# Optimization experiments

Hardware: AMD Instinct MI355X
Metric: run time of the kernel (lower is better)

## Reference

```python
import jax, jax.numpy as jnp
import numpy as np

B, D, O, K = 8192, 256, 256, 16


def setup_inputs() -> dict:
    key = jax.random.key(0)
    k1, k2, k3, k4 = jax.random.split(key, 4)
    x = jax.random.normal(k1, (B, D), dtype=jnp.float32)
    # learned params
    values = jax.random.uniform(k2, (O, D, K), dtype=jnp.float32, minval=-0.05, maxval=0.05)
    skip_w = jax.random.normal(k3, (O, D), dtype=jnp.float32) * (1.0 / np.sqrt(D))
    skip_b = jax.random.uniform(k4, (O,), dtype=jnp.float32, minval=-1.0, maxval=1.0) / np.sqrt(D)
    # fixed buffer (non-trainable)
    grid = jnp.linspace(-1.0, 1.0, K).astype(jnp.float32)
    return {"x": x, "values": values, "skip_w": skip_w, "skip_b": skip_b, "grid": grid}


def reference(x, values, skip_w, skip_b, grid):
    # x: [B, D]; values: [O, D, K]; grid: [K]
    num_knots = grid.shape[0]
    xc = jnp.clip(x, -1.0, 1.0)
    # torch.bucketize(x, grid) (right=False) == searchsorted side='left'
    right = jnp.searchsorted(grid, xc, side="left")            # [B, D]
    left = jnp.clip(right - 1, 0, num_knots - 2)               # [B, D]
    right = left + 1
    g0 = grid[left]
    g1 = grid[right]
    w = (xc - g0) / (g1 - g0 + 1e-12)                          # [B, D]
    # sparse linear-interp coefficients over knots: 2 nonzeros per (b, d)
    coeff = (1.0 - w)[..., None] * jax.nn.one_hot(left, num_knots, dtype=xc.dtype) \
          + w[..., None] * jax.nn.one_hot(right, num_knots, dtype=xc.dtype)  # [B, D, K]
    # y[b,o] = sum_d sum_k coeff[b,d,k] * values[o,d,k]  (== per-dim gather+interp+accumulate)
    y = jnp.einsum("bdk,odk->bo", coeff, values)
    y = y + xc @ skip_w.T + skip_b
    return y
```

## Files before the change

kernel.cpp:

```cpp
#include <hip/hip_runtime.h>
#include <hip/hip_bf16.h>
#include <stdint.h>


#define D_DIM  256
#define O_DIM  256
#define BM     64
#define BK     64
#define KS     4
#define ITERS  16
#define NTHR   256

typedef __attribute__((ext_vector_type(8))) short bf16x8;
typedef __attribute__((ext_vector_type(4))) float f32x4;

__global__ __launch_bounds__(256) void kan_prep(
    const float* __restrict__ values,
    const float* __restrict__ skip_w,
    const float* __restrict__ gknots,
    const float* __restrict__ x,
    unsigned short* __restrict__ Vp)
{
    int tid = blockIdx.x * blockDim.x + threadIdx.x;
    int e = tid * 8;
    int o = e >> 12;
    int kflat = e & 4095;
    float sw = skip_w[(o << 8) | (kflat >> 4)];
    int kmod = kflat & 15;

    const float4* vp4 = reinterpret_cast<const float4*>(values + e);
    float4 v0 = vp4[0], v1 = vp4[1];
    float f[8] = {v0.x, v0.y, v0.z, v0.w, v1.x, v1.y, v1.z, v1.w};
    unsigned int w[4];
#pragma unroll
    for (int j = 0; j < 4; ++j) {
        float2 ab;
        ab.x = f[2*j]     + gknots[kmod + 2*j]     * sw;
        ab.y = f[2*j + 1] + gknots[kmod + 2*j + 1] * sw;
        __hip_bfloat162 p2 = __float22bfloat162_rn(ab);
        __builtin_memcpy(&w[j], &p2, 4);
    }
    size_t c = (size_t)(kflat >> 3) * 256 + (size_t)o;
    *reinterpret_cast<uint4*>(Vp + c * 8) = make_uint4(w[0], w[1], w[2], w[3]);

    {
        int pb = (int)blockIdx.x;
        int mt = (pb & 7) + 8 * ((pb >> 3) & 15);
        int rowbase = mt * BM + (pb >> 7) * 16;
        int t = (int)threadIdx.x;
        const float4* xw = reinterpret_cast<const float4*>(
            x + (size_t)(rowbase + (t >> 4)) * D_DIM) + (t & 15) * 4;
        float s = 0.f;
#pragma unroll
        for (int k = 0; k < 4; ++k) {
            float4 v = xw[k];
            s += v.x + v.y + v.z + v.w;
        }
        asm volatile("" :: "v"(s));
    }
}

__global__ __launch_bounds__(NTHR, 2) void kan_gemm(
    const float* __restrict__ x,
    const unsigned short* __restrict__ Vp,
    float* __restrict__ part,
    float* __restrict__ out)
{
    __shared__ unsigned short As[4][2][64 * 64];

    const int t    = threadIdx.x;
    const int lane = t & 63;
    const int wid  = t >> 6;
    const int l15  = lane & 15;
    const int lhi  = lane >> 4;

    const int bid = (int)blockIdx.x;
    const int m8  = bid & 7;
    const int ks  = (bid >> 3) & 3;
    const int mhi = bid >> 5;
    const int mt  = m8 + 8 * mhi;
    const int bm0 = mt * BM;
    const size_t kc0 = (size_t)ks * 128;

    const float* xr = x + (size_t)(bm0 + lane) * D_DIM + ks * 64;

    char* abase[2] = { (char*)&As[wid][0][0] + lane * 128,
                       (char*)&As[wid][1][0] + lane * 128 };
    const int lsw = lane & 7;

    auto stageA = [&](int buf, float4 xv) {
        float vv[4] = {xv.x, xv.y, xv.z, xv.w};
        char* base = abase[buf];
#pragma unroll
        for (int d = 0; d < 4; ++d) {
            float xc = fminf(1.f, fmaxf(-1.f, vv[d]));
            float tt = (xc + 1.f) * 7.5f;
            int li = (int)tt;
            li = li > 14 ? 14 : li;
            float w1 = tt - (float)li;
            float2 cw; cw.x = 1.f - w1; cw.y = w1;
            __hip_bfloat162 p2 = __float22bfloat162_rn(cw);
            unsigned int pk;
            __builtin_memcpy(&pk, &p2, 4);
            unsigned long long w64 = (unsigned long long)pk << ((li & 1) * 16);
            unsigned int lo = (unsigned int)w64;
            unsigned int hi = (unsigned int)(w64 >> 32);
            int jl = li >> 1;
            unsigned int wd[8];
#pragma unroll
            for (int j = 0; j < 8; ++j)
                wd[j] = (j == jl) ? lo : ((j == jl + 1) ? hi : 0u);
            *reinterpret_cast<uint4*>(base + (((2 * d)     ^ lsw) << 4)) =
                make_uint4(wd[0], wd[1], wd[2], wd[3]);
            *reinterpret_cast<uint4*>(base + (((2 * d + 1) ^ lsw) << 4)) =
                make_uint4(wd[4], wd[5], wd[6], wd[7]);
        }
    };

    #define LOADB(BG, KT)                                                      \
        {                                                                      \
            const unsigned short* _b =                                         \
                Vp + (kc0 + (size_t)(KT) * 8) * 2048;                          \
            _Pragma("unroll")                                                  \
            for (int kh = 0; kh < 2; ++kh)                                     \
                _Pragma("unroll")                                              \
                for (int ni = 0; ni < 4; ++ni) {                               \
                    int n = wid * 64 + ni * 16 + l15;                          \
                    BG[kh * 4 + ni] = *reinterpret_cast<const bf16x8*>(        \
                        _b + ((size_t)((kh * 4 + lhi) * 256 + n)) * 8);        \
                }                                                              \
        }

    f32x4 acc[4][4] = {};
    bf16x8 bgA[8], bgB[8], bgC[8];

    int abyte[4];
#pragma unroll
    for (int mi = 0; mi < 4; ++mi) abyte[mi] = (mi * 16 + l15) * 128;
    const int a7 = l15 & 7;

    float4 xcur = *reinterpret_cast<const float4*>(xr);
    LOADB(bgA, 0)
    LOADB(bgB, 1)
    stageA(0, xcur);
    float4 xn = *reinterpret_cast<const float4*>(xr + 4);

    #define IT(KT, CUR, BGC_, BGN2)                                            \
        {                                                                      \
            const bool last = (KT) == ITERS - 1;                               \
            if ((KT) + 2 < ITERS) { LOADB(BGN2, (KT) + 2) }                    \
            const char* Ab = (const char*)&As[wid][CUR][0];                    \
            bf16x8 af[4];                                                      \
                                                                   \
            _Pragma("unroll")                                                  \
            for (int mi = 0; mi < 4; ++mi)                                     \
                af[mi] = *reinterpret_cast<const bf16x8*>(                     \
                    Ab + abyte[mi] + ((lhi ^ a7) << 4));                       \
            __builtin_amdgcn_s_setprio(1);                                     \
            _Pragma("unroll")                                                  \
            for (int mi = 0; mi < 4; ++mi)                                     \
                _Pragma("unroll")                                              \
                for (int ni = 0; ni < 4; ++ni)                                 \
                    acc[mi][ni] = __builtin_amdgcn_mfma_f32_16x16x32_bf16(     \
                        af[mi], BGC_[ni], acc[mi][ni], 0, 0, 0);               \
            __builtin_amdgcn_s_setprio(0);                                     \
                                    \
            if (!last) {                                                       \
                stageA((CUR) ^ 1, xn);                                         \
                if ((KT) + 2 < ITERS)                                          \
                    xn = *reinterpret_cast<const float4*>(xr + ((KT) + 2) * 4);\
            }                                                                  \
                                                                   \
            _Pragma("unroll")                                                  \
            for (int mi = 0; mi < 4; ++mi)                                     \
                af[mi] = *reinterpret_cast<const bf16x8*>(                     \
                    Ab + abyte[mi] + (((4 + lhi) ^ a7) << 4));                 \
            __builtin_amdgcn_s_setprio(1);                                     \
            _Pragma("unroll")                                                  \
            for (int mi = 0; mi < 4; ++mi)                                     \
                _Pragma("unroll")                                              \
                for (int ni = 0; ni < 4; ++ni)                                 \
                    acc[mi][ni] = __builtin_amdgcn_mfma_f32_16x16x32_bf16(     \
                        af[mi], BGC_[4 + ni], acc[mi][ni], 0, 0, 0);           \
            __builtin_amdgcn_s_setprio(0);                                     \
        }

    IT(0, 0, bgA, bgC)  IT(1, 1, bgB, bgA)  IT(2, 0, bgC, bgB)
    IT(3, 1, bgA, bgC)  IT(4, 0, bgB, bgA)  IT(5, 1, bgC, bgB)
    IT(6, 0, bgA, bgC)  IT(7, 1, bgB, bgA)  IT(8, 0, bgC, bgB)
    IT(9, 1, bgA, bgC)  IT(10, 0, bgB, bgA) IT(11, 1, bgC, bgB)
    IT(12, 0, bgA, bgC) IT(13, 1, bgB, bgA) IT(14, 0, bgC, bgB)
    IT(15, 1, bgA, bgC)
    #undef IT
    #undef LOADB

    float* dst = (ks == 0) ? out : part + (size_t)(ks - 1) * (8192 * 256);
#pragma unroll
    for (int ni = 0; ni < 4; ++ni) {
        int col = wid * 64 + ni * 16 + l15;
#pragma unroll
        for (int mi = 0; mi < 4; ++mi) {
            f32x4 v = acc[mi][ni];
            int row0 = bm0 + mi * 16 + lhi * 4;
#pragma unroll
            for (int r = 0; r < 4; ++r)
                dst[(size_t)(row0 + r) * O_DIM + col] = v[r];
        }
    }
}

__global__ __launch_bounds__(256) void kan_reduce(
    const float* __restrict__ part,
    const float* __restrict__ skip_b,
    float* __restrict__ out)
{
    int rbid = (int)blockIdx.x;
    int c    = rbid & 7;
    int tq   = rbid >> 3;
    int mhi  = tq >> 4;
    int sub  = tq & 15;
    int mt   = c + 8 * mhi;
    int row0 = mt * BM + sub * 4;

    int i   = (int)threadIdx.x;
    int row = row0 + (i >> 6);
    int col = (i & 63) * 4;
    size_t e = (size_t)row * O_DIM + col;

    f32x4 s = *reinterpret_cast<const f32x4*>(out + e);
    s += *reinterpret_cast<const f32x4*>(skip_b + col);
    s += *reinterpret_cast<const f32x4*>(part + e);
    s += *reinterpret_cast<const f32x4*>(part + (size_t)8192 * 256 + e);
    s += *reinterpret_cast<const f32x4*>(part + (size_t)2 * 8192 * 256 + e);
    *reinterpret_cast<f32x4*>(out + e) = s;
}

__global__ __launch_bounds__(256) void kan_naive(
    const float* __restrict__ x,
    const unsigned short* __restrict__ Vp,
    const float* __restrict__ skip_b,
    float* __restrict__ out)
{
    int b = blockIdx.x, o = threadIdx.x;
    float acc = skip_b[o];
    for (int d = 0; d < 256; ++d) {
        float xc = fminf(1.f, fmaxf(-1.f, x[(size_t)b * 256 + d]));
        float tt = (xc + 1.f) * 7.5f;
        int li = (int)tt; li = li > 14 ? 14 : li;
        float w1 = tt - (float)li;
        int k0 = d * 16 + li;
        unsigned short u0 = Vp[((size_t)(k0 >> 3) * 256 + o) * 8 + (k0 & 7)];
        int k1 = k0 + 1;
        unsigned short u1 = Vp[((size_t)(k1 >> 3) * 256 + o) * 8 + (k1 & 7)];
        float f0 = __uint_as_float((unsigned)u0 << 16);
        float f1 = __uint_as_float((unsigned)u1 << 16);
        acc += (1.f - w1) * f0 + w1 * f1;
    }
    out[(size_t)b * 256 + o] = acc;
}

extern "C" void kernel_launch(void* const* d_in, const int* in_sizes, int n_in,
                              void* d_out, int out_size, void* d_ws, size_t ws_size,
                              hipStream_t stream) {
    const float* x      = (const float*)d_in[0];
    const float* values = (const float*)d_in[1];
    const float* skip_w = (const float*)d_in[2];
    const float* skip_b = (const float*)d_in[3];
    const float* gknots = (const float*)d_in[4];
    float* out = (float*)d_out;
    (void)in_sizes; (void)n_in; (void)out_size;

    unsigned short* Vp = (unsigned short*)d_ws;
    float* part = (float*)((char*)d_ws + 2u * 1024 * 1024);

    kan_prep<<<dim3(512), dim3(256), 0, stream>>>(values, skip_w, gknots, x, Vp);

    const size_t need = 2u * 1024 * 1024
                      + (size_t)3 * 8192 * 256 * sizeof(float);
    if (ws_size >= need) {
        kan_gemm<<<dim3(512), dim3(NTHR), 0, stream>>>(x, Vp, part, out);
        kan_reduce<<<dim3(2048), dim3(256), 0, stream>>>(part, skip_b, out);
    } else {
        kan_naive<<<dim3(8192), dim3(256), 0, stream>>>(x, Vp, skip_b, out);
    }
}
```

Baseline: 42.13 us.

## Build interpolation A-fragments directly in registers instead of staging through LDS

Each lane now loads the x values it needs for its own MFMA A-fragment rows and builds the sparse bf16 interpolation coefficients in registers. This removes the shared-memory staging buffer, the LDS writes and reads, and the per-row lane mapping. The cost is redundant coefficient work, since several lanes recompute fragments from the same x elements. Global x loads become four strided rows per lane, and the occupancy hint is dropped from the launch bounds.

Result: slower. 75.70 us (+79.7%).

```diff
diff --git a/kernel.cpp b/kernel.cpp
--- a/kernel.cpp
+++ b/kernel.cpp
@@ -6,7 +6,6 @@
 #define D_DIM  256
 #define O_DIM  256
 #define BM     64
-#define BK     64
 #define KS     4
 #define ITERS  16
 #define NTHR   256
@@ -60,19 +59,19 @@
     }
 }
 
-__global__ __launch_bounds__(NTHR, 2) void kan_gemm(
+__global__ __launch_bounds__(NTHR) void kan_gemm(
     const float* __restrict__ x,
     const unsigned short* __restrict__ Vp,
     float* __restrict__ part,
     float* __restrict__ out)
 {
-    __shared__ unsigned short As[4][2][64 * 64];
-
     const int t    = threadIdx.x;
     const int lane = t & 63;
     const int wid  = t >> 6;
     const int l15  = lane & 15;
     const int lhi  = lane >> 4;
+    const int hi2  = lhi >> 1;
+    const int jbase = (lhi & 1) * 4;
 
     const int bid = (int)blockIdx.x;
     const int m8  = bid & 7;
@@ -82,39 +81,33 @@
     const int bm0 = mt * BM;
     const size_t kc0 = (size_t)ks * 128;
 
-    const float* xr = x + (size_t)(bm0 + lane) * D_DIM + ks * 64;
-
-    char* abase[2] = { (char*)&As[wid][0][0] + lane * 128,
-                       (char*)&As[wid][1][0] + lane * 128 };
-    const int lsw = lane & 7;
-
-    auto stageA = [&](int buf, float4 xv) {
-        float vv[4] = {xv.x, xv.y, xv.z, xv.w};
-        char* base = abase[buf];
-#pragma unroll
-        for (int d = 0; d < 4; ++d) {
-            float xc = fminf(1.f, fmaxf(-1.f, vv[d]));
-            float tt = (xc + 1.f) * 7.5f;
-            int li = (int)tt;
-            li = li > 14 ? 14 : li;
-            float w1 = tt - (float)li;
-            float2 cw; cw.x = 1.f - w1; cw.y = w1;
-            __hip_bfloat162 p2 = __float22bfloat162_rn(cw);
-            unsigned int pk;
-            __builtin_memcpy(&pk, &p2, 4);
-            unsigned long long w64 = (unsigned long long)pk << ((li & 1) * 16);
-            unsigned int lo = (unsigned int)w64;
-            unsigned int hi = (unsigned int)(w64 >> 32);
-            int jl = li >> 1;
-            unsigned int wd[8];
-#pragma unroll
-            for (int j = 0; j < 8; ++j)
-                wd[j] = (j == jl) ? lo : ((j == jl + 1) ? hi : 0u);
-            *reinterpret_cast<uint4*>(base + (((2 * d)     ^ lsw) << 4)) =
-                make_uint4(wd[0], wd[1], wd[2], wd[3]);
-            *reinterpret_cast<uint4*>(base + (((2 * d + 1) ^ lsw) << 4)) =
-                make_uint4(wd[4], wd[5], wd[6], wd[7]);
-        }
+    const float* xrow[4];
+#pragma unroll
+    for (int mi = 0; mi < 4; ++mi)
+        xrow[mi] = x + (size_t)(bm0 + mi * 16 + l15) * D_DIM + ks * 64;
+
+    auto mkfrag = [&](float xv) -> bf16x8 {
+        float xc = fminf(1.f, fmaxf(-1.f, xv));
+        float tt = (xc + 1.f) * 7.5f;
+        int li = (int)tt;
+        li = li > 14 ? 14 : li;
+        float w1 = tt - (float)li;
+        float2 cw; cw.x = 1.f - w1; cw.y = w1;
+        __hip_bfloat162 p2 = __float22bfloat162_rn(cw);
+        unsigned int pk;
+        __builtin_memcpy(&pk, &p2, 4);
+        unsigned long long w64 = (unsigned long long)pk << ((li & 1) << 4);
+        unsigned int lo = (unsigned int)w64;
+        unsigned int hi = (unsigned int)(w64 >> 32);
+        int jl = (li >> 1) - jbase;
+        uint4 w;
+        w.x = (jl == 0) ? lo : ((jl == -1) ? hi : 0u);
+        w.y = (jl == 1) ? lo : ((jl == 0)  ? hi : 0u);
+        w.z = (jl == 2) ? lo : ((jl == 1)  ? hi : 0u);
+        w.w = (jl == 3) ? lo : ((jl == 2)  ? hi : 0u);
+        bf16x8 r;
+        __builtin_memcpy(&r, &w, 16);
+        return r;
     };
 
     #define LOADB(BG, KT)                                                      \
@@ -131,31 +124,30 @@
                 }                                                              \
         }
 
+    #define LOADX(XV, KT)                                                      \
+        {                                                                      \
+            _Pragma("unroll")                                                  \
+            for (int mi = 0; mi < 4; ++mi)                                     \
+                XV[mi] = *reinterpret_cast<const float4*>(xrow[mi] + (KT) * 4);\
+        }
+
     f32x4 acc[4][4] = {};
     bf16x8 bgA[8], bgB[8], bgC[8];
-
-    int abyte[4];
-#pragma unroll
-    for (int mi = 0; mi < 4; ++mi) abyte[mi] = (mi * 16 + l15) * 128;
-    const int a7 = l15 & 7;
-
-    float4 xcur = *reinterpret_cast<const float4*>(xr);
+    float4 xA[4], xB[4];
+
     LOADB(bgA, 0)
     LOADB(bgB, 1)
-    stageA(0, xcur);
-    float4 xn = *reinterpret_cast<const float4*>(xr + 4);
-
-    #define IT(KT, CUR, BGC_, BGN2)                                            \
+    LOADX(xA, 0)
+    LOADX(xB, 1)
+
+    #define IT(KT, BGC_, BGN2, XC, XN)                                         \
         {                                                                      \
-            const bool last = (KT) == ITERS - 1;                               \
             if ((KT) + 2 < ITERS) { LOADB(BGN2, (KT) + 2) }                    \
-            const char* Ab = (const char*)&As[wid][CUR][0];                    \
             bf16x8 af[4];                                                      \
-                                                                   \
-            _Pragma("unroll")                                                  \
-            for (int mi = 0; mi < 4; ++mi)                                     \
-                af[mi] = *reinterpret_cast<const bf16x8*>(                     \
-                    Ab + abyte[mi] + ((lhi ^ a7) << 4));                       \
+                                                   \
+            _Pragma("unroll")                                                  \
+            for (int mi = 0; mi < 4; ++mi)                                     \
+                af[mi] = mkfrag(hi2 ? XC[mi].y : XC[mi].x);                    \
             __builtin_amdgcn_s_setprio(1);                                     \
             _Pragma("unroll")                                                  \
             for (int mi = 0; mi < 4; ++mi)                                     \
@@ -164,17 +156,11 @@
                     acc[mi][ni] = __builtin_amdgcn_mfma_f32_16x16x32_bf16(     \
                         af[mi], BGC_[ni], acc[mi][ni], 0, 0, 0);               \
             __builtin_amdgcn_s_setprio(0);                                     \
-                                    \
-            if (!last) {                                                       \
-                stageA((CUR) ^ 1, xn);                                         \
-                if ((KT) + 2 < ITERS)                                          \
-                    xn = *reinterpret_cast<const float4*>(xr + ((KT) + 2) * 4);\
-            }                                                                  \
-                                                                   \
-            _Pragma("unroll")                                                  \
-            for (int mi = 0; mi < 4; ++mi)                                     \
-                af[mi] = *reinterpret_cast<const bf16x8*>(                     \
-                    Ab + abyte[mi] + (((4 + lhi) ^ a7) << 4));                 \
+                                               \
+            _Pragma("unroll")                                                  \
+            for (int mi = 0; mi < 4; ++mi)                                     \
+                af[mi] = mkfrag(hi2 ? XC[mi].w : XC[mi].z);                    \
+            if ((KT) + 2 < ITERS) { LOADX(XC, (KT) + 2) }                      \
             __builtin_amdgcn_s_setprio(1);                                     \
             _Pragma("unroll")                                                  \
             for (int mi = 0; mi < 4; ++mi)                                     \
@@ -185,14 +171,15 @@
             __builtin_amdgcn_s_setprio(0);                                     \
         }
 
-    IT(0, 0, bgA, bgC)  IT(1, 1, bgB, bgA)  IT(2, 0, bgC, bgB)
-    IT(3, 1, bgA, bgC)  IT(4, 0, bgB, bgA)  IT(5, 1, bgC, bgB)
-    IT(6, 0, bgA, bgC)  IT(7, 1, bgB, bgA)  IT(8, 0, bgC, bgB)
-    IT(9, 1, bgA, bgC)  IT(10, 0, bgB, bgA) IT(11, 1, bgC, bgB)
-    IT(12, 0, bgA, bgC) IT(13, 1, bgB, bgA) IT(14, 0, bgC, bgB)
-    IT(15, 1, bgA, bgC)
+    IT(0,  bgA, bgC, xA, xB)  IT(1,  bgB, bgA, xB, xA)  IT(2,  bgC, bgB, xA, xB)
+    IT(3,  bgA, bgC, xB, xA)  IT(4,  bgB, bgA, xA, xB)  IT(5,  bgC, bgB, xB, xA)
+    IT(6,  bgA, bgC, xA, xB)  IT(7,  bgB, bgA, xB, xA)  IT(8,  bgC, bgB, xA, xB)
+    IT(9,  bgA, bgC, xB, xA)  IT(10, bgB, bgA, xA, xB)  IT(11, bgC, bgB, xB, xA)
+    IT(12, bgA, bgC, xA, xB)  IT(13, bgB, bgA, xB, xA)  IT(14, bgC, bgB, xA, xB)
+    IT(15, bgA, bgC, xB, xA)
     #undef IT
     #undef LOADB
+    #undef LOADX
 
     float* dst = (ks == 0) ? out : part + (size_t)(ks - 1) * (8192 * 256);
 #pragma unroll
```
